# Kernel optimization log

Hardware: AMD Instinct MI355X
Metric: run time of the kernel (lower is better)

## Reference

```python
import jax, jax.numpy as jnp
import numpy as np

EPS = 1e-8  # torch.nn.CosineSimilarity default eps


def setup_inputs() -> dict:
    key = jax.random.key(0)
    k1, k2 = jax.random.split(key)
    N, C, K = 131072, 128, 512
    embeddings = jax.random.normal(k1, (N, C), dtype=jnp.float32)
    prototypes = jax.random.normal(k2, (K, C), dtype=jnp.float32)
    return {"embeddings": embeddings, "prototypes": prototypes}


def reference(embeddings, prototypes):
    # Cosine similarity between each embedding and each prototype, expressed as
    # a normalized GEMM instead of the O(N*K*C) broadcast the torch code builds.
    e = embeddings / jnp.maximum(
        jnp.linalg.norm(embeddings, axis=-1, keepdims=True), EPS)
    p = prototypes / jnp.maximum(
        jnp.linalg.norm(prototypes, axis=-1, keepdims=True), EPS)
    cos = jnp.einsum('nc,kc->nk', e, p)  # (N, K)
    dists = 1.0 - cos
    scores = -(dists * dists)
    return scores
```

## Files before the change

kernel.cpp:

```cpp
#include <hip/hip_runtime.h>

#define EPS_F 1e-8f

typedef float  f32x4  __attribute__((ext_vector_type(4)));
typedef __bf16 bf16x8 __attribute__((ext_vector_type(8)));
typedef unsigned short u16x4 __attribute__((ext_vector_type(4)));

__device__ inline unsigned short f2bf(float x) {
  unsigned int u = __float_as_uint(x);
  u += 0x7fffu + ((u >> 16) & 1u);
  return (unsigned short)(u >> 16);
}

__global__ __launch_bounds__(256) void hproto_kernel(
    const float* __restrict__ emb, const float* __restrict__ proto,
    float* __restrict__ out)
{
  constexpr int CD = 128;
  constexpr int KP = 512;
  constexpr int BM = 128;
  constexpr int BN = 128;

  __shared__ unsigned short sA[BM * CD];
  __shared__ unsigned short sB[BN * CD];
  __shared__ float rne[BM];
  __shared__ float rnp[BN];

  const int tid  = threadIdx.x;
  const int lane = tid & 63;
  const int wave = tid >> 6;
  const long brow = (long)blockIdx.x * BM;

  auto stage = [&](const float* __restrict__ src, unsigned short* dst, float* rn) {
    const float4* s4 = (const float4*)src;
    #pragma unroll
    for (int s = 0; s < 16; ++s) {
      int f  = s * 256 + tid;
      int r  = f >> 5;
      int c4 = f & 31;
      float4 v = s4[f];
      float ss = v.x*v.x + v.y*v.y + v.z*v.z + v.w*v.w;
      #pragma unroll
      for (int m = 16; m >= 1; m >>= 1) ss += __shfl_xor(ss, m);
      if ((tid & 31) == 0) rn[r] = 1.0f / fmaxf(sqrtf(ss), EPS_F);
      u16x4 b;
      b[0] = f2bf(v.x); b[1] = f2bf(v.y); b[2] = f2bf(v.z); b[3] = f2bf(v.w);
      int idx = (r * CD + c4 * 4) ^ ((r & 7) << 3);
      *(u16x4*)&dst[idx] = b;
    }
  };

  stage(emb + brow * CD, sA, rne);
  stage(proto, sB, rnp);
  __syncthreads();

  const int wr = (wave >> 1) * 64;
  const int wc = (wave & 1) * 64;

  for (int c = 0; c < 4; ++c) {
    f32x4 acc[4][4];
    #pragma unroll
    for (int m = 0; m < 4; ++m)
      #pragma unroll
      for (int n = 0; n < 4; ++n) acc[m][n] = f32x4{0.f, 0.f, 0.f, 0.f};

    #pragma unroll
    for (int kk = 0; kk < 4; ++kk) {
      const int k0 = kk * 32 + (lane >> 4) * 8;
      bf16x8 af[4], bfr[4];
      #pragma unroll
      for (int m = 0; m < 4; ++m) {
        int row = wr + m * 16 + (lane & 15);
        int idx = (row * CD + k0) ^ ((row & 7) << 3);
        af[m] = *(const bf16x8*)&sA[idx];
      }
      #pragma unroll
      for (int n = 0; n < 4; ++n) {
        int col = wc + n * 16 + (lane & 15);
        int idx = (col * CD + k0) ^ ((col & 7) << 3);
        bfr[n] = *(const bf16x8*)&sB[idx];
      }
      #pragma unroll
      for (int m = 0; m < 4; ++m)
        #pragma unroll
        for (int n = 0; n < 4; ++n)
          acc[m][n] = __builtin_amdgcn_mfma_f32_16x16x32_bf16(af[m], bfr[n], acc[m][n], 0, 0, 0);
    }

    #pragma unroll
    for (int m = 0; m < 4; ++m) {
      float re[4];
      #pragma unroll
      for (int j = 0; j < 4; ++j) re[j] = rne[wr + m * 16 + (lane >> 4) * 4 + j];
      #pragma unroll
      for (int n = 0; n < 4; ++n) {
        float rp = rnp[wc + n * 16 + (lane & 15)];
        long col = (long)c * BN + wc + n * 16 + (lane & 15);
        #pragma unroll
        for (int j = 0; j < 4; ++j) {
          long row = brow + wr + m * 16 + (lane >> 4) * 4 + j;
          float cs = acc[m][n][j] * re[j] * rp;
          float d  = 1.0f - cs;
          out[row * KP + col] = -(d * d);
        }
      }
    }

    if (c < 3) {
      __syncthreads();
      stage(proto + (long)(c + 1) * BN * CD, sB, rnp);
      __syncthreads();
    }
  }
}

extern "C" void kernel_launch(void* const* d_in, const int* in_sizes, int n_in,
                              void* d_out, int out_size, void* d_ws, size_t ws_size,
                              hipStream_t stream) {
  const float* emb   = (const float*)d_in[0];
  const float* proto = (const float*)d_in[1];
  float* out = (float*)d_out;
  const int C = 128;
  const int N = in_sizes[0] / C;
  hproto_kernel<<<N / 128, 256, 0, stream>>>(emb, proto, out);
}
```

Baseline: 420.3 us.

## Pre-normalize prototypes to bf16 in a separate kernel and read B fragments from global

Adds a small prekernel that normalizes the prototypes and converts them to bf16 in workspace. The main kernel then loads B fragments straight from global (L2-resident) into registers instead of restaging the prototypes into shared memory per column chunk. This removes four redundant prototype stagings per block, their fp32->bf16 conversions, and the barriers around them. It also uses nontemporal stores for the large output and hoists the embedding norms into registers. The cost is higher register pressure from holding 16 B fragments, plus a second kernel launch.

```diff
diff --git a/kernel.cpp b/kernel.cpp
--- a/kernel.cpp
+++ b/kernel.cpp
@@ -12,27 +12,41 @@
   return (unsigned short)(u >> 16);
 }
 
+__global__ __launch_bounds__(256) void proto_norm_kernel(
+    const float* __restrict__ proto, unsigned short* __restrict__ Bn)
+{
+  const int tid = threadIdx.x;
+  const int g   = tid & 31;
+  const int row = blockIdx.x * 8 + (tid >> 5);
+  const float4 v = *(const float4*)&proto[row * 128 + g * 4];
+  float ss = v.x*v.x + v.y*v.y + v.z*v.z + v.w*v.w;
+  #pragma unroll
+  for (int m = 16; m >= 1; m >>= 1) ss += __shfl_xor(ss, m);
+  const float rn = 1.0f / fmaxf(sqrtf(ss), EPS_F);
+  u16x4 b;
+  b[0] = f2bf(v.x * rn); b[1] = f2bf(v.y * rn);
+  b[2] = f2bf(v.z * rn); b[3] = f2bf(v.w * rn);
+  *(u16x4*)&Bn[row * 128 + g * 4] = b;
+}
+
 __global__ __launch_bounds__(256) void hproto_kernel(
-    const float* __restrict__ emb, const float* __restrict__ proto,
+    const float* __restrict__ emb, const unsigned short* __restrict__ Bn,
     float* __restrict__ out)
 {
   constexpr int CD = 128;
   constexpr int KP = 512;
   constexpr int BM = 128;
-  constexpr int BN = 128;
 
   __shared__ unsigned short sA[BM * CD];
-  __shared__ unsigned short sB[BN * CD];
   __shared__ float rne[BM];
-  __shared__ float rnp[BN];
 
   const int tid  = threadIdx.x;
   const int lane = tid & 63;
   const int wave = tid >> 6;
   const long brow = (long)blockIdx.x * BM;
 
-  auto stage = [&](const float* __restrict__ src, unsigned short* dst, float* rn) {
-    const float4* s4 = (const float4*)src;
+  {
+    const float4* s4 = (const float4*)(emb + brow * CD);
     #pragma unroll
     for (int s = 0; s < 16; ++s) {
       int f  = s * 256 + tid;
@@ -42,22 +56,38 @@
       float ss = v.x*v.x + v.y*v.y + v.z*v.z + v.w*v.w;
       #pragma unroll
       for (int m = 16; m >= 1; m >>= 1) ss += __shfl_xor(ss, m);
-      if ((tid & 31) == 0) rn[r] = 1.0f / fmaxf(sqrtf(ss), EPS_F);
+      if ((tid & 31) == 0) rne[r] = 1.0f / fmaxf(sqrtf(ss), EPS_F);
       u16x4 b;
       b[0] = f2bf(v.x); b[1] = f2bf(v.y); b[2] = f2bf(v.z); b[3] = f2bf(v.w);
       int idx = (r * CD + c4 * 4) ^ ((r & 7) << 3);
-      *(u16x4*)&dst[idx] = b;
+      *(u16x4*)&sA[idx] = b;
     }
-  };
-
-  stage(emb + brow * CD, sA, rne);
-  stage(proto, sB, rnp);
+  }
   __syncthreads();
 
   const int wr = (wave >> 1) * 64;
   const int wc = (wave & 1) * 64;
+  const int hi = lane >> 4;
+  const int lo = lane & 15;
 
+  f32x4 re[4];
+  #pragma unroll
+  for (int m = 0; m < 4; ++m)
+    re[m] = *(const f32x4*)&rne[wr + m * 16 + hi * 4];
+
+  float* const obase = out + (brow + wr + hi * 4) * KP + wc + lo;
+
+  #pragma unroll 1
   for (int c = 0; c < 4; ++c) {
+    bf16x8 bfr[4][4];
+    #pragma unroll
+    for (int n = 0; n < 4; ++n) {
+      const unsigned short* bp = Bn + (c * 128 + wc + n * 16 + lo) * CD + hi * 8;
+      #pragma unroll
+      for (int kk = 0; kk < 4; ++kk)
+        bfr[kk][n] = *(const bf16x8*)(bp + kk * 32);
+    }
+
     f32x4 acc[4][4];
     #pragma unroll
     for (int m = 0; m < 4; ++m)
@@ -66,50 +96,34 @@
 
     #pragma unroll
     for (int kk = 0; kk < 4; ++kk) {
-      const int k0 = kk * 32 + (lane >> 4) * 8;
-      bf16x8 af[4], bfr[4];
+      const int k0 = kk * 32 + hi * 8;
+      bf16x8 af[4];
       #pragma unroll
       for (int m = 0; m < 4; ++m) {
-        int row = wr + m * 16 + (lane & 15);
+        int row = wr + m * 16 + lo;
         int idx = (row * CD + k0) ^ ((row & 7) << 3);
         af[m] = *(const bf16x8*)&sA[idx];
-      }
-      #pragma unroll
-      for (int n = 0; n < 4; ++n) {
-        int col = wc + n * 16 + (lane & 15);
-        int idx = (col * CD + k0) ^ ((col & 7) << 3);
-        bfr[n] = *(const bf16x8*)&sB[idx];
       }
       #pragma unroll
       for (int m = 0; m < 4; ++m)
         #pragma unroll
         for (int n = 0; n < 4; ++n)
-          acc[m][n] = __builtin_amdgcn_mfma_f32_16x16x32_bf16(af[m], bfr[n], acc[m][n], 0, 0, 0);
+          acc[m][n] = __builtin_amdgcn_mfma_f32_16x16x32_bf16(af[m], bfr[kk][n], acc[m][n], 0, 0, 0);
     }
 
+    float* const oc = obase + c * 128;
     #pragma unroll
     for (int m = 0; m < 4; ++m) {
-      float re[4];
       #pragma unroll
-      for (int j = 0; j < 4; ++j) re[j] = rne[wr + m * 16 + (lane >> 4) * 4 + j];
-      #pragma unroll
-      for (int n = 0; n < 4; ++n) {
-        float rp = rnp[wc + n * 16 + (lane & 15)];
-        long col = (long)c * BN + wc + n * 16 + (lane & 15);
+      for (int j = 0; j < 4; ++j) {
+        float* orow = oc + (long)(m * 16 + j) * KP;
         #pragma unroll
-        for (int j = 0; j < 4; ++j) {
-          long row = brow + wr + m * 16 + (lane >> 4) * 4 + j;
-          float cs = acc[m][n][j] * re[j] * rp;
+        for (int n = 0; n < 4; ++n) {
+          float cs = acc[m][n][j] * re[m][j];
           float d  = 1.0f - cs;
-          out[row * KP + col] = -(d * d);
+          __builtin_nontemporal_store(-(d * d), orow + n * 16);
         }
       }
-    }
-
-    if (c < 3) {
-      __syncthreads();
-      stage(proto + (long)(c + 1) * BN * CD, sB, rnp);
-      __syncthreads();
     }
   }
 }
@@ -120,7 +134,10 @@
   const float* emb   = (const float*)d_in[0];
   const float* proto = (const float*)d_in[1];
   float* out = (float*)d_out;
+  unsigned short* Bn = (unsigned short*)d_ws;
   const int C = 128;
   const int N = in_sizes[0] / C;
-  hproto_kernel<<<N / 128, 256, 0, stream>>>(emb, proto, out);
+  const int K = in_sizes[1] / C;
+  proto_norm_kernel<<<K / 8, 256, 0, stream>>>(proto, Bn);
+  hproto_kernel<<<N / 128, 256, 0, stream>>>(emb, Bn, out);
 }
```

Result: faster. 342.8 us (-18.4%).
